# Optimization experiments

Hardware: AMD Instinct MI355X
Metric: run time of the kernel (lower is better)

The kernel has to match this reference:

```python
import jax, jax.numpy as jnp
import numpy as np

N = 100000   # nodes
E = 1600000  # edges
IN, HID, OUT = 128, 128, 64


def setup_inputs() -> dict:
    key = jax.random.key(0)
    ks = jax.random.split(key, 8)
    x = jax.random.normal(ks[0], (N, IN), dtype=jnp.float32)
    edge_index = jax.random.randint(ks[1], (2, E), 0, N, dtype=jnp.int64)
    W1 = jax.random.normal(ks[2], (IN, HID), dtype=jnp.float32) * 0.05
    b1 = jnp.zeros((HID,), dtype=jnp.float32)
    W2 = jax.random.normal(ks[3], (HID, OUT), dtype=jnp.float32) * 0.05
    b2 = jnp.zeros((OUT,), dtype=jnp.float32)
    Wd = jax.random.normal(ks[4], (OUT, IN), dtype=jnp.float32) * 0.05
    bd = jnp.zeros((IN,), dtype=jnp.float32)
    return {"x": x, "edge_index": edge_index, "W1": W1, "b1": b1,
            "W2": W2, "b2": b2, "Wd": Wd, "bd": bd}


def _gcn_conv(x, src, dst, W, b):
    # PyG GCNConv: add self-loops, symmetric normalization D^-1/2 (A+I) D^-1/2,
    # messages flow src -> dst, aggregated by sum at dst.
    h = x @ W                                   # [N, F]
    ones = jnp.ones((src.shape[0],), x.dtype)
    deg = jax.ops.segment_sum(ones, dst, num_segments=N) + 1.0  # +1 for self-loop
    dinv = jax.lax.rsqrt(deg)                   # deg^-1/2, [N]
    coef = dinv[src] * dinv[dst]                # per-edge norm
    agg = jax.ops.segment_sum(h[src] * coef[:, None], dst, num_segments=N)
    agg = agg + h * (dinv * dinv)[:, None]      # self-loop contribution
    return agg + b


def reference(x, edge_index, W1, b1, W2, b2, Wd, bd):
    src, dst = edge_index[0], edge_index[1]
    h = jax.nn.relu(_gcn_conv(x, src, dst, W1, b1))
    # dropout in eval mode -> identity
    z = _gcn_conv(h, src, dst, W2, b2)          # [N, OUT] embedding
    x_recon = z @ Wd + bd                        # [N, IN]
    return (x_recon, z)
```

## Files before the change

kernel.cpp:

```cpp
#include <hip/hip_runtime.h>
#include <hip/hip_bf16.h>
#include <hip/hip_fp16.h>


#define TPB 256
#define CAP 64
#define BINCAP 220000
#define FILLW 112

typedef float v2f __attribute__((ext_vector_type(2)));


__device__ __forceinline__ unsigned short f2bf(float f) {
    unsigned u = __float_as_uint(f);
    unsigned r = u + 0x7fffu + ((u >> 16) & 1u);
    return (unsigned short)(r >> 16);
}
__device__ __forceinline__ float bf_lo(unsigned u) { return __uint_as_float(u << 16); }
__device__ __forceinline__ float bf_hi(unsigned u) { return __uint_as_float(u & 0xffff0000u); }


template <int K, int C, int TN, bool BIAS, bool INBF, bool OUTBF>
__device__ __forceinline__ void gemm_body(const void* __restrict__ Ap,
                                          const float* __restrict__ W,
                                          const float* __restrict__ bias,
                                          void* __restrict__ outp, int N, int bid,
                                          float* __restrict__ Ws) {
    constexpr int BM  = 128;
    constexpr int TM  = 8;
    constexpr int BK  = 32;
    constexpr int NCT = C / TN;
    static_assert(NCT * (BM / TM) == TPB, "thread layout");

    int tid = threadIdx.x;
    int tc = tid % NCT;
    int tr = tid / NCT;
    int c0 = tc * TN;
    int r0 = bid * BM + tr * TM;

    float acc[TM][TN] = {};

    for (int k0 = 0; k0 < K; k0 += BK) {
        __syncthreads();
        for (int i = tid * 4; i < BK * C; i += TPB * 4)
            *(float4*)&Ws[i] = *(const float4*)&W[k0 * C + i];
        __syncthreads();

        for (int k = 0; k < BK; k += 4) {
            float4 a[TM];
            uint2  au[TM];
#pragma unroll
            for (int i = 0; i < TM; ++i) {
                int r = r0 + i;
                if (r >= N) r = N - 1;
                if (INBF)
                    au[i] = *(const uint2*)((const unsigned short*)Ap + (size_t)r * K + k0 + k);
                else
                    a[i] = *(const float4*)((const float*)Ap + (size_t)r * K + k0 + k);
            }
#pragma unroll
            for (int kk = 0; kk < 4; ++kk) {
                float w[TN];
#pragma unroll
                for (int j = 0; j < TN; j += 4)
                    *(float4*)&w[j] = *(const float4*)&Ws[(k + kk) * C + c0 + j];
#pragma unroll
                for (int i = 0; i < TM; ++i) {
                    float av;
                    if (INBF) {
                        unsigned uu = (kk < 2) ? au[i].x : au[i].y;
                        av = (kk & 1) ? bf_hi(uu) : bf_lo(uu);
                    } else {
                        av = ((const float*)&a[i])[kk];
                    }
#pragma unroll
                    for (int j = 0; j < TN; ++j) acc[i][j] += av * w[j];
                }
            }
        }
    }

#pragma unroll
    for (int i = 0; i < TM; ++i) {
        int r = r0 + i;
        if (r >= N) continue;
        if (BIAS) {
#pragma unroll
            for (int j = 0; j < TN; ++j) acc[i][j] += bias[c0 + j];
        }
        if (OUTBF) {
            unsigned short* ob = (unsigned short*)outp + (size_t)r * C + c0;
            unsigned pk[TN / 2];
#pragma unroll
            for (int j = 0; j < TN; j += 2)
                pk[j / 2] = (unsigned)f2bf(acc[i][j]) | ((unsigned)f2bf(acc[i][j + 1]) << 16);
            if (TN == 8)      *(uint4*)ob = *(uint4*)pk;
            else if (TN == 4) *(uint2*)ob = *(uint2*)pk;
        } else {
            float* of = (float*)outp + (size_t)r * C + c0;
#pragma unroll
            for (int j = 0; j < TN; j += 4)
                *(float4*)&of[j] = *(float4*)&acc[i][j];
        }
    }
}

template <int K, int C, int TN, bool BIAS, bool INBF, bool OUTBF>
__global__ __launch_bounds__(TPB) void gemm_k(const void* __restrict__ Ap,
                                              const float* __restrict__ W,
                                              const float* __restrict__ bias,
                                              void* __restrict__ outp, int N) {
    __shared__ float Ws[32 * C];
    gemm_body<K, C, TN, BIAS, INBF, OUTBF>(Ap, W, bias, outp, N, blockIdx.x, Ws);
}


__global__ __launch_bounds__(TPB) void fused1_k(const float* __restrict__ x,
                                                const float* __restrict__ W1,
                                                unsigned* __restrict__ h1b,
                                                const int* __restrict__ src,
                                                const int* __restrict__ dst,
                                                uint2* __restrict__ binBuf,
                                                int* __restrict__ binCnt,
                                                int N, int E, int gb, unsigned M) {
    __shared__ float Ws[32 * 128];
    __shared__ int hist[8], gbase[8], lpos[8];
    if ((int)blockIdx.x < gb) {
        gemm_body<128, 128, 8, false, false, true>(x, W1, nullptr, h1b, N, blockIdx.x, Ws);
    } else {
        int bid = (int)blockIdx.x - gb;
        int tid = (int)threadIdx.x;
        if (tid < 8) { hist[tid] = 0; lpos[tid] = 0; }
        __syncthreads();

        int e0 = (bid * TPB + tid) * 8;
        int ne = E - e0; ne = ne > 8 ? 8 : (ne < 0 ? 0 : ne);
        int ss[8], dd[8], bb8[8];
        if (ne == 8) {
            int4 sa = *(const int4*)&src[e0];
            int4 sb = *(const int4*)&src[e0 + 4];
            int4 da = *(const int4*)&dst[e0];
            int4 db = *(const int4*)&dst[e0 + 4];
            ss[0]=sa.x; ss[1]=sa.y; ss[2]=sa.z; ss[3]=sa.w;
            ss[4]=sb.x; ss[5]=sb.y; ss[6]=sb.z; ss[7]=sb.w;
            dd[0]=da.x; dd[1]=da.y; dd[2]=da.z; dd[3]=da.w;
            dd[4]=db.x; dd[5]=db.y; dd[6]=db.z; dd[7]=db.w;
        } else {
            for (int q = 0; q < ne; ++q) { ss[q] = src[e0 + q]; dd[q] = dst[e0 + q]; }
        }
        for (int q = 0; q < ne; ++q) {
            bb8[q] = (int)(((unsigned long long)(unsigned)dd[q] * M) >> 32);
            atomicAdd(&hist[bb8[q]], 1);
        }
        __syncthreads();
        if (tid < 8) gbase[tid] = atomicAdd(&binCnt[tid], hist[tid]);
        __syncthreads();
        for (int q = 0; q < ne; ++q) {
            int b = bb8[q];
            int p = gbase[b] + atomicAdd(&lpos[b], 1);
            if (p < BINCAP)
                binBuf[(size_t)b * BINCAP + p] = make_uint2((unsigned)ss[q], (unsigned)dd[q]);
        }
    }
}


__global__ __launch_bounds__(TPB) void fill_k(const uint2* __restrict__ binBuf,
                                              const int* __restrict__ binCnt,
                                              int* __restrict__ cnt,
                                              unsigned* __restrict__ bucket, int N) {
    int bin = (int)blockIdx.x & 7;
    int w   = (int)blockIdx.x >> 3;
    int cb  = binCnt[bin];
    if (cb > BINCAP) cb = BINCAP;
    const uint2* eb = binBuf + (size_t)bin * BINCAP;

    for (int base = w * (TPB * 8); base < cb; base += FILLW * (TPB * 8)) {
        int e0 = base + (int)threadIdx.x * 8;
        if (e0 + 8 <= cb) {
            unsigned s[8], d[8];
#pragma unroll
            for (int q = 0; q < 8; q += 2) {
                uint4 t = *(const uint4*)&eb[e0 + q];
                s[q] = t.x; d[q] = t.y; s[q + 1] = t.z; d[q + 1] = t.w;
            }
            int rr[8];
#pragma unroll
            for (int q = 0; q < 8; ++q) rr[q] = atomicAdd(&cnt[(int)d[q]], 1);
#pragma unroll
            for (int q = 0; q < 8; ++q)
                if (rr[q] < CAP) bucket[(size_t)rr[q] * N + d[q]] = s[q];
        } else {
            int lim = e0 + 8 < cb ? e0 + 8 : cb;
            for (int e = e0; e < lim; ++e) {
                uint2 t = eb[e];
                int r = atomicAdd(&cnt[(int)t.y], 1);
                if (r < CAP) bucket[(size_t)r * N + t.y] = t.x;
            }
        }
    }
}


__global__ __launch_bounds__(TPB) void dinv_k(const int* __restrict__ cnt,
                                              float* __restrict__ dinv, int N) {
    int i = blockIdx.x * TPB + (int)threadIdx.x;
    if (i < N) dinv[i] = rsqrtf((float)cnt[i] + 1.0f);
}


template <int F2, bool RELU, bool OUTBF>
__global__ __launch_bounds__(TPB) void agg_k(const unsigned* __restrict__ h,
                                             const float* __restrict__ dinv,
                                             const int* __restrict__ cnt,
                                             const unsigned* __restrict__ bucket,
                                             const float* __restrict__ bias,
                                             void* __restrict__ outp, int N) {
    constexpr int NPB = TPB / F2;
    int ln = threadIdx.x / F2;
    int f2 = threadIdx.x % F2;
    int n  = blockIdx.x * NPB + ln;
    if (n >= N) return;

    int cfull = cnt[n];
    float di = dinv[n];
    const unsigned* hp = h + f2;
    unsigned us = hp[(size_t)n * F2];
    v2f acc;
    acc.x = bf_lo(us) * (di * di);
    acc.y = bf_hi(us) * (di * di);

    int cn = cfull < CAP ? cfull : CAP;
    const unsigned* bp = bucket + n;

    int nfull = cn & ~7;
    int s[8], sn2[8];
    if (nfull > 0) {
#pragma unroll
        for (int q = 0; q < 8; ++q) s[q] = (int)bp[(size_t)q * N];
    }
    for (int j = 0; j < nfull; ) {
        int jn = j + 8;
        bool more = jn < nfull;
        if (more) {
#pragma unroll
            for (int q = 0; q < 8; ++q) sn2[q] = (int)bp[(size_t)(jn + q) * N];
        }
        unsigned v[8];
        float ds[8];
#pragma unroll
        for (int q = 0; q < 8; ++q) {
            v[q]  = hp[(size_t)s[q] * F2];
            ds[q] = dinv[s[q]];
        }
#pragma unroll
        for (int q = 0; q < 8; ++q) {
            float c = ds[q] * di;
            v2f hv; hv.x = bf_lo(v[q]); hv.y = bf_hi(v[q]);
            acc += hv * c;
        }
        if (more) {
#pragma unroll
            for (int q = 0; q < 8; ++q) s[q] = sn2[q];
        }
        j = jn;
    }
    for (int j = nfull; j < cn; ++j) {
        int sx = (int)bp[(size_t)j * N];
        unsigned v = hp[(size_t)sx * F2];
        float c = dinv[sx] * di;
        acc.x += c * bf_lo(v);
        acc.y += c * bf_hi(v);
    }

    float rx = acc.x + bias[2 * f2];
    float ry = acc.y + bias[2 * f2 + 1];
    if (RELU) { rx = fmaxf(rx, 0.f); ry = fmaxf(ry, 0.f); }
    if (OUTBF) {
        unsigned pk = (unsigned)f2bf(rx) | ((unsigned)f2bf(ry) << 16);
        ((unsigned*)outp)[(size_t)n * F2 + f2] = pk;
    } else {
        v2f r; r.x = rx; r.y = ry;
        __builtin_nontemporal_store(r, (v2f*)outp + (size_t)n * F2 + f2);
    }
}


extern "C" void kernel_launch(void* const* d_in, const int* in_sizes, int n_in,
                              void* d_out, int out_size, void* d_ws, size_t ws_size,
                              hipStream_t stream) {
    const float* x    = (const float*)d_in[0];
    const int*   eidx = (const int*)d_in[1];
    const float* W1   = (const float*)d_in[2];
    const float* b1   = (const float*)d_in[3];
    const float* W2   = (const float*)d_in[4];
    const float* b2   = (const float*)d_in[5];
    const float* Wd   = (const float*)d_in[6];
    const float* bd   = (const float*)d_in[7];

    const int N = in_sizes[0] / 128;
    const int E = in_sizes[1] / 2;
    const int* src = eidx;
    const int* dst = eidx + E;

    size_t off = 0;
    auto alloc = [&](size_t bytes) {
        void* p = (char*)d_ws + off;
        off += (bytes + 255) & ~(size_t)255;
        return p;
    };
    int*      cnt     = (int*)alloc((size_t)N * 4);
    float*    dinv    = (float*)alloc((size_t)N * 4);
    unsigned* bucket  = (unsigned*)alloc((size_t)N * CAP * 4);
    unsigned* h1b     = (unsigned*)alloc((size_t)N * 64 * 4);
    unsigned* h2b     = (unsigned*)alloc((size_t)N * 32 * 4);
    unsigned* hrelu_b = (unsigned*)alloc((size_t)N * 64 * 4);
    int*      binCnt  = (int*)alloc(256);
    uint2*    binBuf  = (uint2*)hrelu_b;
    (void)ws_size;

    float* x_recon = (float*)d_out;
    float* z_out   = (float*)d_out + (size_t)N * 128;

    const int gb = (N + 127) / 128;
    const int bb = (E + TPB * 8 - 1) / (TPB * 8);
    const unsigned M = (unsigned)((8ULL << 32) / (unsigned)N);

    (void)hipMemsetAsync(cnt, 0, (size_t)N * 4, stream);
    (void)hipMemsetAsync(binCnt, 0, 256, stream);

    fused1_k<<<gb + bb, TPB, 0, stream>>>(x, W1, h1b, src, dst, binBuf, binCnt, N, E, gb, M);
    fill_k<<<8 * FILLW, TPB, 0, stream>>>(binBuf, binCnt, cnt, bucket, N);
    dinv_k<<<(N + TPB - 1) / TPB, TPB, 0, stream>>>(cnt, dinv, N);

    agg_k<64, true, true><<<(N + 3) / 4, TPB, 0, stream>>>(h1b, dinv, cnt, bucket, b1, hrelu_b, N);
    gemm_k<128, 64, 4, false, true, true><<<gb, TPB, 0, stream>>>(hrelu_b, W2, nullptr, h2b, N);
    agg_k<32, false, false><<<(N + 7) / 8, TPB, 0, stream>>>(h2b, dinv, cnt, bucket, b2, z_out, N);
    gemm_k<64, 128, 8, true, false, false><<<gb, TPB, 0, stream>>>(z_out, Wd, bd, x_recon, N);
}
```

Measured before the change: 470.2 us.

## Fuse aggregation kernels with the following dense GEMMs via shared-memory rows

The layer-1 aggregation (with bias and ReLU) now computes the W2 projection in the same kernel from a per-block shared-memory row buffer, writing h2 directly. The layer-2 aggregation likewise computes the decoder GEMM with Wd and bd from shared memory, writing x_recon. This removes the hrelu round trip, the z reload and two launches. The cost is per-node GEMMs that read W from global/L1 without tiling, which is much less reuse-efficient than the tiled GEMM, and binBuf now needs its own workspace allocation.

```diff
diff --git a/kernel.cpp b/kernel.cpp
--- a/kernel.cpp
+++ b/kernel.cpp
@@ -103,15 +103,6 @@
                 *(float4*)&of[j] = *(float4*)&acc[i][j];
         }
     }
-}
-
-template <int K, int C, int TN, bool BIAS, bool INBF, bool OUTBF>
-__global__ __launch_bounds__(TPB) void gemm_k(const void* __restrict__ Ap,
-                                              const float* __restrict__ W,
-                                              const float* __restrict__ bias,
-                                              void* __restrict__ outp, int N) {
-    __shared__ float Ws[32 * C];
-    gemm_body<K, C, TN, BIAS, INBF, OUTBF>(Ap, W, bias, outp, N, blockIdx.x, Ws);
 }
 
 
@@ -209,79 +200,184 @@
 }
 
 
-template <int F2, bool RELU, bool OUTBF>
-__global__ __launch_bounds__(TPB) void agg_k(const unsigned* __restrict__ h,
-                                             const float* __restrict__ dinv,
-                                             const int* __restrict__ cnt,
-                                             const unsigned* __restrict__ bucket,
-                                             const float* __restrict__ bias,
-                                             void* __restrict__ outp, int N) {
-    constexpr int NPB = TPB / F2;
-    int ln = threadIdx.x / F2;
-    int f2 = threadIdx.x % F2;
+__global__ __launch_bounds__(TPB) void aggG1_k(const unsigned* __restrict__ h,
+                                               const float* __restrict__ dinv,
+                                               const int* __restrict__ cnt,
+                                               const unsigned* __restrict__ bucket,
+                                               const float* __restrict__ b1,
+                                               const float* __restrict__ W2,
+                                               unsigned* __restrict__ h2b, int N) {
+    constexpr int F2 = 64, NPB = TPB / F2;
+    __shared__ float zl[NPB][128];
+    int tid = (int)threadIdx.x;
+    int ln = tid / F2;
+    int f2 = tid % F2;
     int n  = blockIdx.x * NPB + ln;
-    if (n >= N) return;
-
-    int cfull = cnt[n];
-    float di = dinv[n];
-    const unsigned* hp = h + f2;
-    unsigned us = hp[(size_t)n * F2];
-    v2f acc;
-    acc.x = bf_lo(us) * (di * di);
-    acc.y = bf_hi(us) * (di * di);
-
-    int cn = cfull < CAP ? cfull : CAP;
-    const unsigned* bp = bucket + n;
-
-    int nfull = cn & ~7;
-    int s[8], sn2[8];
-    if (nfull > 0) {
-#pragma unroll
-        for (int q = 0; q < 8; ++q) s[q] = (int)bp[(size_t)q * N];
-    }
-    for (int j = 0; j < nfull; ) {
-        int jn = j + 8;
-        bool more = jn < nfull;
-        if (more) {
-#pragma unroll
-            for (int q = 0; q < 8; ++q) sn2[q] = (int)bp[(size_t)(jn + q) * N];
-        }
-        unsigned v[8];
-        float ds[8];
-#pragma unroll
-        for (int q = 0; q < 8; ++q) {
-            v[q]  = hp[(size_t)s[q] * F2];
-            ds[q] = dinv[s[q]];
-        }
-#pragma unroll
-        for (int q = 0; q < 8; ++q) {
-            float c = ds[q] * di;
-            v2f hv; hv.x = bf_lo(v[q]); hv.y = bf_hi(v[q]);
-            acc += hv * c;
-        }
-        if (more) {
-#pragma unroll
-            for (int q = 0; q < 8; ++q) s[q] = sn2[q];
-        }
-        j = jn;
-    }
-    for (int j = nfull; j < cn; ++j) {
-        int sx = (int)bp[(size_t)j * N];
-        unsigned v = hp[(size_t)sx * F2];
-        float c = dinv[sx] * di;
-        acc.x += c * bf_lo(v);
-        acc.y += c * bf_hi(v);
-    }
-
-    float rx = acc.x + bias[2 * f2];
-    float ry = acc.y + bias[2 * f2 + 1];
-    if (RELU) { rx = fmaxf(rx, 0.f); ry = fmaxf(ry, 0.f); }
-    if (OUTBF) {
-        unsigned pk = (unsigned)f2bf(rx) | ((unsigned)f2bf(ry) << 16);
-        ((unsigned*)outp)[(size_t)n * F2 + f2] = pk;
-    } else {
+
+    if (n < N) {
+        int cfull = cnt[n];
+        float di = dinv[n];
+        const unsigned* hp = h + f2;
+        unsigned us = hp[(size_t)n * F2];
+        v2f acc;
+        acc.x = bf_lo(us) * (di * di);
+        acc.y = bf_hi(us) * (di * di);
+
+        int cn = cfull < CAP ? cfull : CAP;
+        const unsigned* bp = bucket + n;
+
+        int nfull = cn & ~7;
+        int s[8], sn2[8];
+        if (nfull > 0) {
+#pragma unroll
+            for (int q = 0; q < 8; ++q) s[q] = (int)bp[(size_t)q * N];
+        }
+        for (int j = 0; j < nfull; ) {
+            int jn = j + 8;
+            bool more = jn < nfull;
+            if (more) {
+#pragma unroll
+                for (int q = 0; q < 8; ++q) sn2[q] = (int)bp[(size_t)(jn + q) * N];
+            }
+            unsigned v[8];
+            float ds[8];
+#pragma unroll
+            for (int q = 0; q < 8; ++q) {
+                v[q]  = hp[(size_t)s[q] * F2];
+                ds[q] = dinv[s[q]];
+            }
+#pragma unroll
+            for (int q = 0; q < 8; ++q) {
+                float c = ds[q] * di;
+                v2f hv; hv.x = bf_lo(v[q]); hv.y = bf_hi(v[q]);
+                acc += hv * c;
+            }
+            if (more) {
+#pragma unroll
+                for (int q = 0; q < 8; ++q) s[q] = sn2[q];
+            }
+            j = jn;
+        }
+        for (int j = nfull; j < cn; ++j) {
+            int sx = (int)bp[(size_t)j * N];
+            unsigned v = hp[(size_t)sx * F2];
+            float c = dinv[sx] * di;
+            acc.x += c * bf_lo(v);
+            acc.y += c * bf_hi(v);
+        }
+
+        float rx = fmaxf(acc.x + b1[2 * f2], 0.f);
+        float ry = fmaxf(acc.y + b1[2 * f2 + 1], 0.f);
+        zl[ln][2 * f2]     = rx;
+        zl[ln][2 * f2 + 1] = ry;
+    }
+    __syncthreads();
+
+    int dn = tid / 64;
+    int c  = tid & 63;
+    int nn = blockIdx.x * NPB + dn;
+    if (nn < N) {
+        float a = 0.f;
+        const float* w = W2 + c;
+#pragma unroll 8
+        for (int k = 0; k < 128; ++k) a += zl[dn][k] * w[(size_t)k * 64];
+        float b = __shfl_down(a, 1);
+        if ((c & 1) == 0) {
+            unsigned pk = (unsigned)f2bf(a) | ((unsigned)f2bf(b) << 16);
+            h2b[(size_t)nn * 32 + (c >> 1)] = pk;
+        }
+    }
+}
+
+
+__global__ __launch_bounds__(TPB) void agg2g_k(const unsigned* __restrict__ h,
+                                               const float* __restrict__ dinv,
+                                               const int* __restrict__ cnt,
+                                               const unsigned* __restrict__ bucket,
+                                               const float* __restrict__ bias,
+                                               const float* __restrict__ Wd,
+                                               const float* __restrict__ bd,
+                                               float* __restrict__ z_out,
+                                               float* __restrict__ x_recon, int N) {
+    constexpr int F2 = 32, NPB = TPB / F2;
+    __shared__ float zl[NPB][64];
+    int ln = (int)threadIdx.x / F2;
+    int f2 = (int)threadIdx.x % F2;
+    int n  = blockIdx.x * NPB + ln;
+
+    if (n < N) {
+        int cfull = cnt[n];
+        float di = dinv[n];
+        const unsigned* hp = h + f2;
+        unsigned us = hp[(size_t)n * F2];
+        v2f acc;
+        acc.x = bf_lo(us) * (di * di);
+        acc.y = bf_hi(us) * (di * di);
+
+        int cn = cfull < CAP ? cfull : CAP;
+        const unsigned* bp = bucket + n;
+
+        int nfull = cn & ~7;
+        int s[8], sn2[8];
+        if (nfull > 0) {
+#pragma unroll
+            for (int q = 0; q < 8; ++q) s[q] = (int)bp[(size_t)q * N];
+        }
+        for (int j = 0; j < nfull; ) {
+            int jn = j + 8;
+            bool more = jn < nfull;
+            if (more) {
+#pragma unroll
+                for (int q = 0; q < 8; ++q) sn2[q] = (int)bp[(size_t)(jn + q) * N];
+            }
+            unsigned v[8];
+            float ds[8];
+#pragma unroll
+            for (int q = 0; q < 8; ++q) {
+                v[q]  = hp[(size_t)s[q] * F2];
+                ds[q] = dinv[s[q]];
+            }
+#pragma unroll
+            for (int q = 0; q < 8; ++q) {
+                float c = ds[q] * di;
+                v2f hv; hv.x = bf_lo(v[q]); hv.y = bf_hi(v[q]);
+                acc += hv * c;
+            }
+            if (more) {
+#pragma unroll
+                for (int q = 0; q < 8; ++q) s[q] = sn2[q];
+            }
+            j = jn;
+        }
+        for (int j = nfull; j < cn; ++j) {
+            int sx = (int)bp[(size_t)j * N];
+            unsigned v = hp[(size_t)sx * F2];
+            float c = dinv[sx] * di;
+            acc.x += c * bf_lo(v);
+            acc.y += c * bf_hi(v);
+        }
+
+        float rx = acc.x + bias[2 * f2];
+        float ry = acc.y + bias[2 * f2 + 1];
         v2f r; r.x = rx; r.y = ry;
-        __builtin_nontemporal_store(r, (v2f*)outp + (size_t)n * F2 + f2);
+        __builtin_nontemporal_store(r, (v2f*)z_out + (size_t)n * F2 + f2);
+        *(v2f*)&zl[ln][2 * f2] = r;
+    }
+    __syncthreads();
+
+    int dn = (int)threadIdx.x / 32;
+    int c0 = ((int)threadIdx.x % 32) * 4;
+    int nn = blockIdx.x * NPB + dn;
+    if (nn < N) {
+        float a0 = bd[c0], a1 = bd[c0 + 1], a2 = bd[c0 + 2], a3 = bd[c0 + 3];
+#pragma unroll 4
+        for (int k = 0; k < 64; ++k) {
+            float zv = zl[dn][k];
+            float4 w = *(const float4*)&Wd[k * 128 + c0];
+            a0 += zv * w.x; a1 += zv * w.y; a2 += zv * w.z; a3 += zv * w.w;
+        }
+        float4 o; o.x = a0; o.y = a1; o.z = a2; o.w = a3;
+        *(float4*)&x_recon[(size_t)nn * 128 + c0] = o;
     }
 }
 
@@ -314,9 +410,8 @@
     unsigned* bucket  = (unsigned*)alloc((size_t)N * CAP * 4);
     unsigned* h1b     = (unsigned*)alloc((size_t)N * 64 * 4);
     unsigned* h2b     = (unsigned*)alloc((size_t)N * 32 * 4);
-    unsigned* hrelu_b = (unsigned*)alloc((size_t)N * 64 * 4);
+    uint2*    binBuf  = (uint2*)alloc((size_t)8 * BINCAP * 8);
     int*      binCnt  = (int*)alloc(256);
-    uint2*    binBuf  = (uint2*)hrelu_b;
     (void)ws_size;
 
     float* x_recon = (float*)d_out;
@@ -333,8 +428,7 @@
     fill_k<<<8 * FILLW, TPB, 0, stream>>>(binBuf, binCnt, cnt, bucket, N);
     dinv_k<<<(N + TPB - 1) / TPB, TPB, 0, stream>>>(cnt, dinv, N);
 
-    agg_k<64, true, true><<<(N + 3) / 4, TPB, 0, stream>>>(h1b, dinv, cnt, bucket, b1, hrelu_b, N);
-    gemm_k<128, 64, 4, false, true, true><<<gb, TPB, 0, stream>>>(hrelu_b, W2, nullptr, h2b, N);
-    agg_k<32, false, false><<<(N + 7) / 8, TPB, 0, stream>>>(h2b, dinv, cnt, bucket, b2, z_out, N);
-    gemm_k<64, 128, 8, true, false, false><<<gb, TPB, 0, stream>>>(z_out, Wd, bd, x_recon, N);
-}
+    aggG1_k<<<(N + 3) / 4, TPB, 0, stream>>>(h1b, dinv, cnt, bucket, b1, W2, h2b, N);
+    agg2g_k<<<(N + 7) / 8, TPB, 0, stream>>>(h2b, dinv, cnt, bucket, b2, Wd, bd,
+                                             z_out, x_recon, N);
+}
```

Result: slower. 538.2 us (+14.5%).
